# Performance work log

Measured on AMD Instinct MI355X. Metric: run time of the kernel, lower is better.

Reference implementation:

```python
import jax, jax.numpy as jnp
import numpy as np

B, T, E, H = 8, 1024, 1024, 16
D = E // H  # head_dim = 64


def setup_inputs() -> dict:
    key = jax.random.key(0)
    ks = jax.random.split(key, 11)
    s = 1.0 / np.sqrt(E)
    inp = {
        'query': jax.random.normal(ks[0], (B, T, E), jnp.float32),
        'key': jax.random.normal(ks[1], (B, T, E), jnp.float32),
        'value': jax.random.normal(ks[2], (B, T, E), jnp.float32),
        'Wq': jax.random.uniform(ks[3], (E, E), jnp.float32, -s, s),
        'bq': jax.random.uniform(ks[4], (E,), jnp.float32, -s, s),
        'Wk': jax.random.uniform(ks[5], (E, E), jnp.float32, -s, s),
        'bk': jax.random.uniform(ks[6], (E,), jnp.float32, -s, s),
        'Wv': jax.random.uniform(ks[7], (E, E), jnp.float32, -s, s),
        'bv': jax.random.uniform(ks[8], (E,), jnp.float32, -s, s),
        'Wo': jax.random.uniform(ks[9], (E, E), jnp.float32, -s, s),
        'bo': jax.random.uniform(ks[10], (E,), jnp.float32, -s, s),
    }
    return inp


def reference(query, key, value, Wq, bq, Wk, bk, Wv, bv, Wo, bo):
    scale = np.sqrt(D).astype(np.float32)
    # projections: Linear applies x @ W.T + b (torch convention); W shape (out,in)
    q = (query @ Wq.T + bq).reshape(B, T, H, D).transpose(0, 2, 1, 3)  # (B,H,Tq,D)
    k = (key @ Wk.T + bk).reshape(B, T, H, D).transpose(0, 2, 1, 3)    # (B,H,Tk,D)
    v = (value @ Wv.T + bv).reshape(B, T, H, D).transpose(0, 2, 1, 3)  # (B,H,Tk,D)
    scores = jnp.einsum('bhqd,bhkd->bhqk', q, k) / scale
    attn = jax.nn.softmax(scores, axis=-1)  # dropout = identity (eval)
    out = jnp.einsum('bhqk,bhkd->bhqd', attn, v)
    out = out.transpose(0, 2, 1, 3).reshape(B, T, E)
    return out @ Wo.T + bo
```

## Files before the change

### kernel.cpp

```cpp
#include <hip/hip_runtime.h>
#include <stdint.h>

#define BB 8
#define TT 1024
#define EE 1024
#define HH 16
#define DD 64

typedef __attribute__((ext_vector_type(8))) __bf16 bf16x8;
typedef __attribute__((ext_vector_type(4))) float f32x4;
typedef __attribute__((ext_vector_type(4))) unsigned short ushort4v;
typedef __attribute__((ext_vector_type(4))) unsigned int uint4v;

__device__ __forceinline__ unsigned short f2bf(float f) {
  unsigned int u = __float_as_uint(f);
  u += 0x7fffu + ((u >> 16) & 1u);
  return (unsigned short)(u >> 16);
}

__device__ __forceinline__ unsigned int pk2(float a, float b) {
  return ((unsigned int)f2bf(b) << 16) | (unsigned int)f2bf(a);
}

__device__ __forceinline__ f32x4 mfma_16x16x32(bf16x8 a, bf16x8 b, f32x4 c) {
  return __builtin_amdgcn_mfma_f32_16x16x32_bf16(a, b, c, 0, 0, 0);
}

__device__ __forceinline__ void async_ld16(const unsigned short* g, unsigned short* l) {
  __builtin_amdgcn_global_load_lds(
      (const __attribute__((address_space(1))) void*)g,
      (__attribute__((address_space(3))) void*)l, 16, 0, 0);
}

__global__ __launch_bounds__(256) void cast_all(
    const float* __restrict__ xq, const float* __restrict__ xk, const float* __restrict__ xv,
    const float* __restrict__ wq, const float* __restrict__ wk,
    const float* __restrict__ wv, const float* __restrict__ wo,
    unsigned short* __restrict__ ws) {
  int blk = blockIdx.x;
  const float* src; size_t dstoff; int rel;
  if (blk < 4096)       { src = xq; dstoff = 0;        rel = blk; }
  else if (blk < 8192)  { src = xk; dstoff = 8388608;  rel = blk - 4096; }
  else if (blk < 12288) { src = xv; dstoff = 16777216; rel = blk - 8192; }
  else if (blk < 12800) { src = wq; dstoff = 25165824; rel = blk - 12288; }
  else if (blk < 13312) { src = wk; dstoff = 26214400; rel = blk - 12800; }
  else if (blk < 13824) { src = wv; dstoff = 27262976; rel = blk - 13312; }
  else                  { src = wo; dstoff = 28311552; rel = blk - 13824; }
  size_t base = (size_t)rel * 2048 + (size_t)threadIdx.x * 8;
  float4 a = *(const float4*)(src + base);
  float4 b = *(const float4*)(src + base + 4);
  ushort4v o0, o1;
  o0.x = f2bf(a.x); o0.y = f2bf(a.y); o0.z = f2bf(a.z); o0.w = f2bf(a.w);
  o1.x = f2bf(b.x); o1.y = f2bf(b.y); o1.z = f2bf(b.z); o1.w = f2bf(b.w);
  *(ushort4v*)(ws + dstoff + base) = o0;
  *(ushort4v*)(ws + dstoff + base + 4) = o1;
}

template <int OMODE, int AMODE>
__global__ __launch_bounds__(256) void gemm_bt(
    const unsigned short* __restrict__ A, const unsigned short* __restrict__ Wm,
    const float* __restrict__ bias, void* __restrict__ Cout, float scale) {
  const int tid = threadIdx.x;
  const int wave = tid >> 6, lane = tid & 63;
  const int quad = lane >> 4, l16 = lane & 15;
  const int wr = wave >> 1, wc = wave & 1;
  const int n0 = blockIdx.x * 128;
  const int m0 = blockIdx.y * 128;

  __shared__ __align__(16) unsigned short As[128 * 64];
  __shared__ __align__(16) unsigned short Bs[128 * 64];

  const unsigned short* Wb = Wm + (size_t)n0 * 1024 +
                             (OMODE == 2 ? (size_t)blockIdx.z * 1048576 : (size_t)0);

  f32x4 acc[4][4];
#pragma unroll
  for (int i = 0; i < 4; ++i)
#pragma unroll
    for (int j = 0; j < 4; ++j) acc[i][j] = (f32x4){0.f, 0.f, 0.f, 0.f};

  const int row_s = tid >> 3, kc_s = (tid & 7) * 8;
  for (int kt = 0; kt < 16; ++kt) {
    const unsigned short* Akt;
    if (AMODE == 0)
      Akt = A + (size_t)m0 * 1024 + kt * 64;
    else
      Akt = A + (size_t)(m0 >> 10) * 1048576 + (size_t)kt * 65536 + (size_t)(m0 & 1023) * 64;
    const unsigned short* Wkt = Wb + kt * 64;
    const int arow = (AMODE == 0) ? 1024 : 64;
#pragma unroll
    for (int i = 0; i < 4; ++i) {
      int g = i * 256 + tid;
      int row = row_s + i * 32, kc = kc_s;
      async_ld16(Akt + (size_t)row * arow + kc, As + g * 8);
      async_ld16(Wkt + (size_t)row * 1024 + kc, Bs + g * 8);
    }
    __syncthreads();
#pragma unroll
    for (int ks = 0; ks < 2; ++ks) {
      bf16x8 af[4], bfv[4];
      int ko = ks * 32 + quad * 8;
#pragma unroll
      for (int i = 0; i < 4; ++i)
        af[i] = *(const bf16x8*)(As + (wr * 64 + i * 16 + l16) * 64 + ko);
#pragma unroll
      for (int j = 0; j < 4; ++j)
        bfv[j] = *(const bf16x8*)(Bs + (wc * 64 + j * 16 + l16) * 64 + ko);
#pragma unroll
      for (int i = 0; i < 4; ++i)
#pragma unroll
        for (int j = 0; j < 4; ++j) acc[i][j] = mfma_16x16x32(af[i], bfv[j], acc[i][j]);
    }
    __syncthreads();
  }

  if (OMODE == 2) {
    unsigned short* Co = (unsigned short*)Cout;
    size_t zoff = (size_t)blockIdx.z * 1048576;
    const int nxor = ((((l16 >> 2) + 1) & 2) ? 12 : 0);
#pragma unroll
    for (int i = 0; i < 4; ++i)
#pragma unroll
      for (int r = 0; r < 4; ++r) {
        int m = m0 + wr * 64 + i * 16 + quad * 4 + r;
        float bm = bias[m];
#pragma unroll
        for (int j = 0; j < 4; ++j) {
          int n = (n0 + wc * 64 + j * 16 + l16) ^ nxor;
          Co[zoff + (size_t)m * 1024 + n] = f2bf(acc[i][j][r] + bm);
        }
      }
  } else {
#pragma unroll
    for (int j = 0; j < 4; ++j) {
      int n = n0 + wc * 64 + j * 16 + l16;
      float bn = bias[n];
#pragma unroll
      for (int i = 0; i < 4; ++i)
#pragma unroll
        for (int r = 0; r < 4; ++r) {
          int m = m0 + wr * 64 + i * 16 + quad * 4 + r;
          float v = acc[i][j][r] + bn;
          if (OMODE == 0) {
            ((float*)Cout)[(size_t)m * 1024 + n] = v;
          } else {
            v *= scale;
            int b = m >> 10, t = m & 1023, h = n >> 6, d = n & 63;
            ((unsigned short*)Cout)[((size_t)((b << 4) + h) * 1024 + t) * 64 + d] = f2bf(v);
          }
        }
    }
  }
}

__global__ __launch_bounds__(256) void attn(
    const unsigned short* __restrict__ Q,
    const unsigned short* __restrict__ K,
    const unsigned short* __restrict__ Vt,
    unsigned short* __restrict__ O) {
  const int bh = blockIdx.x;
  const int tid = threadIdx.x;
  const int wave = tid >> 6, lane = tid & 63;
  const int quad = lane >> 4, l16 = lane & 15;
  const int q0 = blockIdx.y * 64 + wave * 16;
  const size_t bhTD = (size_t)bh * (TT * DD);
  const unsigned short* Qb = Q + bhTD;
  const unsigned short* Kb = K + bhTD;
  const unsigned short* Vb = Vt + bhTD;

  __shared__ __align__(16) unsigned short Ks[64 * 64];
  __shared__ __align__(16) unsigned short Vs[64 * 64];

  bf16x8 q_lo = *(const bf16x8*)(Qb + (size_t)(q0 + l16) * 64 + quad * 8);
  bf16x8 q_hi = *(const bf16x8*)(Qb + (size_t)(q0 + l16) * 64 + 32 + quad * 8);

  f32x4 o_acc[4];
#pragma unroll
  for (int dd = 0; dd < 4; ++dd) o_acc[dd] = (f32x4){0.f, 0.f, 0.f, 0.f};
  float psum = 0.f;
  const bool lo_half = (quad < 2);

  const int srow = tid >> 3;
  const int schunk = tid & 7;

  for (int it = 0; it < 16; ++it) {
    const int kv0 = it * 64;
#pragma unroll
    for (int i = 0; i < 2; ++i) {
      int row = srow + i * 32;
      int gc = schunk ^ (row & 7);
      async_ld16(Kb + (size_t)(kv0 + row) * 64 + gc * 8, Ks + (row * 8 + schunk) * 8);
      async_ld16(Vb + (size_t)row * 1024 + kv0 + gc * 8, Vs + (row * 8 + schunk) * 8);
    }
    __syncthreads();
#pragma unroll
    for (int c = 0; c < 2; ++c) {
      const int r0 = c * 32 + l16;
      const int r1 = r0 + 16;
      const int sw = r0 & 7;
      bf16x8 k00 = *(const bf16x8*)(Ks + (r0 * 8 + (quad ^ sw)) * 8);
      bf16x8 k01 = *(const bf16x8*)(Ks + (r0 * 8 + ((quad + 4) ^ sw)) * 8);
      bf16x8 k10 = *(const bf16x8*)(Ks + (r1 * 8 + (quad ^ sw)) * 8);
      bf16x8 k11 = *(const bf16x8*)(Ks + (r1 * 8 + ((quad + 4) ^ sw)) * 8);
      f32x4 f0 = (f32x4){0.f, 0.f, 0.f, 0.f};
      f32x4 f1 = (f32x4){0.f, 0.f, 0.f, 0.f};
      f0 = mfma_16x16x32(k00, q_lo, f0);
      f0 = mfma_16x16x32(k01, q_hi, f0);
      f1 = mfma_16x16x32(k10, q_lo, f1);
      f1 = mfma_16x16x32(k11, q_hi, f1);
      float p0 = __expf(f0[0]), p1 = __expf(f0[1]), p2 = __expf(f0[2]), p3 = __expf(f0[3]);
      float p4 = __expf(f1[0]), p5 = __expf(f1[1]), p6 = __expf(f1[2]), p7 = __expf(f1[3]);
      psum += ((p0 + p1) + (p2 + p3)) + ((p4 + p5) + (p6 + p7));
      unsigned int u01 = pk2(p0, p1), u23 = pk2(p2, p3);
      unsigned int u45 = pk2(p4, p5), u67 = pk2(p6, p7);
      unsigned int pu01 = __shfl_xor(u01, 32), pu23 = __shfl_xor(u23, 32);
      unsigned int pu45 = __shfl_xor(u45, 32), pu67 = __shfl_xor(u67, 32);
      uint4v av;
      av.x = lo_half ? u01 : pu45;
      av.y = lo_half ? u23 : pu67;
      av.z = lo_half ? pu01 : u45;
      av.w = lo_half ? pu23 : u67;
      bf16x8 ap = __builtin_bit_cast(bf16x8, av);
#pragma unroll
      for (int dd = 0; dd < 4; ++dd) {
        int vr = dd * 16 + l16;
        bf16x8 bv = *(const bf16x8*)(Vs + (vr * 8 + ((c * 4 + quad) ^ (vr & 7))) * 8);
        o_acc[dd] = mfma_16x16x32(ap, bv, o_acc[dd]);
      }
    }
    __syncthreads();
  }
  psum += __shfl_xor(psum, 16);
  psum += __shfl_xor(psum, 32);
  float inv = 1.f / psum;
#pragma unroll
  for (int r = 0; r < 4; ++r) {
    float invr = __shfl(inv, (lane & 48) | (quad * 4 + r));
    int trow = q0 + quad * 4 + r;
#pragma unroll
    for (int dd = 0; dd < 4; ++dd)
      O[bhTD + (size_t)trow * 64 + dd * 16 + l16] = f2bf(o_acc[dd][r] * invr);
  }
}

extern "C" void kernel_launch(void* const* d_in, const int* in_sizes, int n_in,
                              void* d_out, int out_size, void* d_ws, size_t ws_size,
                              hipStream_t stream) {
  const float* xq = (const float*)d_in[0];
  const float* xk = (const float*)d_in[1];
  const float* xv = (const float*)d_in[2];
  const float* Wq = (const float*)d_in[3];
  const float* bq = (const float*)d_in[4];
  const float* Wk = (const float*)d_in[5];
  const float* bk = (const float*)d_in[6];
  const float* Wv = (const float*)d_in[7];
  const float* bv = (const float*)d_in[8];
  const float* Wo = (const float*)d_in[9];
  const float* bo = (const float*)d_in[10];

  unsigned short* ws = (unsigned short*)d_ws;
  unsigned short* xq_b = ws;
  unsigned short* xk_b = ws + 8388608;
  unsigned short* xv_b = ws + 16777216;
  unsigned short* wq_b = ws + 25165824;
  unsigned short* wk_b = ws + 26214400;
  unsigned short* wv_b = ws + 27262976;
  unsigned short* wo_b = ws + 28311552;
  unsigned short* Qbuf = ws + 29360128;
  unsigned short* Kbuf = ws + 37748736;
  unsigned short* Vtb  = ws + 46137344;
  unsigned short* Obuf = ws + 54525952;

  cast_all<<<14336, 256, 0, stream>>>(xq, xk, xv, Wq, Wk, Wv, Wo, ws);

  gemm_bt<1, 0><<<dim3(8, 64, 1), 256, 0, stream>>>(xq_b, wq_b, bq, (void*)Qbuf, 0.125f);
  gemm_bt<1, 0><<<dim3(8, 64, 1), 256, 0, stream>>>(xk_b, wk_b, bk, (void*)Kbuf, 1.0f);
  gemm_bt<2, 0><<<dim3(8, 8, 8), 256, 0, stream>>>(wv_b, xv_b, bv, (void*)Vtb, 1.0f);
  attn<<<dim3(128, 16), 256, 0, stream>>>(Qbuf, Kbuf, Vtb, Obuf);
  gemm_bt<0, 1><<<dim3(8, 64, 1), 256, 0, stream>>>(Obuf, wo_b, bo, d_out, 1.0f);
}
```

Measured before the change: 339.2 us.

## Fuse QKV projections into one launch, use exp2 and MFMA row sums

```diff
diff --git a/kernel.cpp b/kernel.cpp
--- a/kernel.cpp
+++ b/kernel.cpp
@@ -6,6 +6,8 @@
 #define EE 1024
 #define HH 16
 #define DD 64
+
+#define L2E8 0.18033688011112042f
 
 typedef __attribute__((ext_vector_type(8))) __bf16 bf16x8;
 typedef __attribute__((ext_vector_type(4))) float f32x4;
@@ -56,10 +58,118 @@
   *(ushort4v*)(ws + dstoff + base + 4) = o1;
 }
 
-template <int OMODE, int AMODE>
-__global__ __launch_bounds__(256) void gemm_bt(
+__global__ __launch_bounds__(256, 3) void fused_proj(
+    const unsigned short* __restrict__ xq, const unsigned short* __restrict__ xk,
+    const unsigned short* __restrict__ xv, const unsigned short* __restrict__ wq,
+    const unsigned short* __restrict__ wk, const unsigned short* __restrict__ wv,
+    const float* __restrict__ bq, const float* __restrict__ bk, const float* __restrict__ bv,
+    unsigned short* __restrict__ Qb, unsigned short* __restrict__ Kb,
+    unsigned short* __restrict__ Vtb) {
+  const int id = blockIdx.x;
+  const int tid = threadIdx.x;
+  const int wave = tid >> 6, lane = tid & 63;
+  const int quad = lane >> 4, l16 = lane & 15;
+  const int wr = wave >> 1, wc = wave & 1;
+
+  const unsigned short *A, *W;
+  const float* bias;
+  int mode, m0, n0;
+  size_t zoff = 0;
+  if (id < 512) {
+    mode = 0; A = xq; W = wq; bias = bq;
+    m0 = (id >> 3) * 128; n0 = (id & 7) * 128;
+  } else if (id < 1024) {
+    int t = id - 512;
+    mode = 1; A = xk; W = wk; bias = bk;
+    m0 = (t >> 3) * 128; n0 = (t & 7) * 128;
+  } else {
+    int t = id - 1024;
+    int z = t >> 6;
+    mode = 2; A = wv; W = xv + (size_t)z * 1048576; bias = bv;
+    m0 = ((t >> 3) & 7) * 128; n0 = (t & 7) * 128;
+    zoff = (size_t)z * 1048576;
+  }
+
+  __shared__ __align__(16) unsigned short As[128 * 64];
+  __shared__ __align__(16) unsigned short Bs[128 * 64];
+
+  const unsigned short* Wb = W + (size_t)n0 * 1024;
+
+  f32x4 acc[4][4];
+#pragma unroll
+  for (int i = 0; i < 4; ++i)
+#pragma unroll
+    for (int j = 0; j < 4; ++j) acc[i][j] = (f32x4){0.f, 0.f, 0.f, 0.f};
+
+  const int row_s = tid >> 3, kc_s = (tid & 7) * 8;
+  for (int kt = 0; kt < 16; ++kt) {
+    const unsigned short* Akt = A + (size_t)m0 * 1024 + kt * 64;
+    const unsigned short* Wkt = Wb + kt * 64;
+#pragma unroll
+    for (int i = 0; i < 4; ++i) {
+      int g = i * 256 + tid;
+      int row = row_s + i * 32;
+      async_ld16(Akt + (size_t)row * 1024 + kc_s, As + g * 8);
+      async_ld16(Wkt + (size_t)row * 1024 + kc_s, Bs + g * 8);
+    }
+    __syncthreads();
+#pragma unroll
+    for (int ks = 0; ks < 2; ++ks) {
+      bf16x8 af[4], bfv[4];
+      int ko = ks * 32 + quad * 8;
+#pragma unroll
+      for (int i = 0; i < 4; ++i)
+        af[i] = *(const bf16x8*)(As + (wr * 64 + i * 16 + l16) * 64 + ko);
+#pragma unroll
+      for (int j = 0; j < 4; ++j)
+        bfv[j] = *(const bf16x8*)(Bs + (wc * 64 + j * 16 + l16) * 64 + ko);
+#pragma unroll
+      for (int i = 0; i < 4; ++i)
+#pragma unroll
+        for (int j = 0; j < 4; ++j) acc[i][j] = mfma_16x16x32(af[i], bfv[j], acc[i][j]);
+    }
+    __syncthreads();
+  }
+
+  if (mode == 2) {
+    size_t base = zoff;
+    const int nxor = ((((l16 >> 2) + 1) & 2) ? 12 : 0);
+#pragma unroll
+    for (int i = 0; i < 4; ++i)
+#pragma unroll
+      for (int r = 0; r < 4; ++r) {
+        int m = m0 + wr * 64 + i * 16 + quad * 4 + r;
+        float bm = bias[m];
+#pragma unroll
+        for (int j = 0; j < 4; ++j) {
+          int n = (n0 + wc * 64 + j * 16 + l16) ^ nxor;
+          Vtb[base + (size_t)m * 1024 + n] = f2bf(acc[i][j][r] + bm);
+        }
+      }
+  } else {
+    unsigned short* Out = (mode == 0) ? Qb : Kb;
+    const float scale = (mode == 0) ? L2E8 : 1.0f;
+#pragma unroll
+    for (int j = 0; j < 4; ++j) {
+      int n = n0 + wc * 64 + j * 16 + l16;
+      float bn = bias[n];
+      int h = n >> 6, d = n & 63;
+#pragma unroll
+      for (int i = 0; i < 4; ++i)
+#pragma unroll
+        for (int r = 0; r < 4; ++r) {
+          int m = m0 + wr * 64 + i * 16 + quad * 4 + r;
+          int b = m >> 10, t = m & 1023;
+          float v = (acc[i][j][r] + bn) * scale;
+          Out[((size_t)((b << 4) + h) * 1024 + t) * 64 + d] = f2bf(v);
+        }
+    }
+  }
+}
+
+__global__ __launch_bounds__(256) void gemm_out(
     const unsigned short* __restrict__ A, const unsigned short* __restrict__ Wm,
-    const float* __restrict__ bias, void* __restrict__ Cout, float scale) {
+    const float* __restrict__ bias, float* __restrict__ Cout) {
   const int tid = threadIdx.x;
   const int wave = tid >> 6, lane = tid & 63;
   const int quad = lane >> 4, l16 = lane & 15;
@@ -70,8 +180,7 @@
   __shared__ __align__(16) unsigned short As[128 * 64];
   __shared__ __align__(16) unsigned short Bs[128 * 64];
 
-  const unsigned short* Wb = Wm + (size_t)n0 * 1024 +
-                             (OMODE == 2 ? (size_t)blockIdx.z * 1048576 : (size_t)0);
+  const unsigned short* Wb = Wm + (size_t)n0 * 1024;
 
   f32x4 acc[4][4];
 #pragma unroll
@@ -81,19 +190,15 @@
 
   const int row_s = tid >> 3, kc_s = (tid & 7) * 8;
   for (int kt = 0; kt < 16; ++kt) {
-    const unsigned short* Akt;
-    if (AMODE == 0)
-      Akt = A + (size_t)m0 * 1024 + kt * 64;
-    else
-      Akt = A + (size_t)(m0 >> 10) * 1048576 + (size_t)kt * 65536 + (size_t)(m0 & 1023) * 64;
+    const unsigned short* Akt =
+        A + (size_t)(m0 >> 10) * 1048576 + (size_t)kt * 65536 + (size_t)(m0 & 1023) * 64;
     const unsigned short* Wkt = Wb + kt * 64;
-    const int arow = (AMODE == 0) ? 1024 : 64;
 #pragma unroll
     for (int i = 0; i < 4; ++i) {
       int g = i * 256 + tid;
-      int row = row_s + i * 32, kc = kc_s;
-      async_ld16(Akt + (size_t)row * arow + kc, As + g * 8);
-      async_ld16(Wkt + (size_t)row * 1024 + kc, Bs + g * 8);
+      int row = row_s + i * 32;
+      async_ld16(Akt + (size_t)row * 64 + kc_s, As + g * 8);
+      async_ld16(Wkt + (size_t)row * 1024 + kc_s, Bs + g * 8);
     }
     __syncthreads();
 #pragma unroll
@@ -114,42 +219,17 @@
     __syncthreads();
   }
 
-  if (OMODE == 2) {
-    unsigned short* Co = (unsigned short*)Cout;
-    size_t zoff = (size_t)blockIdx.z * 1048576;
-    const int nxor = ((((l16 >> 2) + 1) & 2) ? 12 : 0);
+#pragma unroll
+  for (int j = 0; j < 4; ++j) {
+    int n = n0 + wc * 64 + j * 16 + l16;
+    float bn = bias[n];
 #pragma unroll
     for (int i = 0; i < 4; ++i)
 #pragma unroll
       for (int r = 0; r < 4; ++r) {
         int m = m0 + wr * 64 + i * 16 + quad * 4 + r;
-        float bm = bias[m];
-#pragma unroll
-        for (int j = 0; j < 4; ++j) {
-          int n = (n0 + wc * 64 + j * 16 + l16) ^ nxor;
-          Co[zoff + (size_t)m * 1024 + n] = f2bf(acc[i][j][r] + bm);
-        }
+        Cout[(size_t)m * 1024 + n] = acc[i][j][r] + bn;
       }
-  } else {
-#pragma unroll
-    for (int j = 0; j < 4; ++j) {
-      int n = n0 + wc * 64 + j * 16 + l16;
-      float bn = bias[n];
-#pragma unroll
-      for (int i = 0; i < 4; ++i)
-#pragma unroll
-        for (int r = 0; r < 4; ++r) {
-          int m = m0 + wr * 64 + i * 16 + quad * 4 + r;
-          float v = acc[i][j][r] + bn;
-          if (OMODE == 0) {
-            ((float*)Cout)[(size_t)m * 1024 + n] = v;
-          } else {
-            v *= scale;
-            int b = m >> 10, t = m & 1023, h = n >> 6, d = n & 63;
-            ((unsigned short*)Cout)[((size_t)((b << 4) + h) * 1024 + t) * 64 + d] = f2bf(v);
-          }
-        }
-    }
   }
 }
 
@@ -174,10 +254,13 @@
   bf16x8 q_lo = *(const bf16x8*)(Qb + (size_t)(q0 + l16) * 64 + quad * 8);
   bf16x8 q_hi = *(const bf16x8*)(Qb + (size_t)(q0 + l16) * 64 + 32 + quad * 8);
 
+  uint4v ou; ou.x = ou.y = ou.z = ou.w = 0x3F803F80u;
+  const bf16x8 ones = __builtin_bit_cast(bf16x8, ou);
+
   f32x4 o_acc[4];
 #pragma unroll
   for (int dd = 0; dd < 4; ++dd) o_acc[dd] = (f32x4){0.f, 0.f, 0.f, 0.f};
-  float psum = 0.f;
+  f32x4 acc5 = (f32x4){0.f, 0.f, 0.f, 0.f};
   const bool lo_half = (quad < 2);
 
   const int srow = tid >> 3;
@@ -208,9 +291,10 @@
       f0 = mfma_16x16x32(k01, q_hi, f0);
       f1 = mfma_16x16x32(k10, q_lo, f1);
       f1 = mfma_16x16x32(k11, q_hi, f1);
-      float p0 = __expf(f0[0]), p1 = __expf(f0[1]), p2 = __expf(f0[2]), p3 = __expf(f0[3]);
-      float p4 = __expf(f1[0]), p5 = __expf(f1[1]), p6 = __expf(f1[2]), p7 = __expf(f1[3]);
-      psum += ((p0 + p1) + (p2 + p3)) + ((p4 + p5) + (p6 + p7));
+      float p0 = __builtin_amdgcn_exp2f(f0[0]), p1 = __builtin_amdgcn_exp2f(f0[1]);
+      float p2 = __builtin_amdgcn_exp2f(f0[2]), p3 = __builtin_amdgcn_exp2f(f0[3]);
+      float p4 = __builtin_amdgcn_exp2f(f1[0]), p5 = __builtin_amdgcn_exp2f(f1[1]);
+      float p6 = __builtin_amdgcn_exp2f(f1[2]), p7 = __builtin_amdgcn_exp2f(f1[3]);
       unsigned int u01 = pk2(p0, p1), u23 = pk2(p2, p3);
       unsigned int u45 = pk2(p4, p5), u67 = pk2(p6, p7);
       unsigned int pu01 = __shfl_xor(u01, 32), pu23 = __shfl_xor(u23, 32);
@@ -221,6 +305,7 @@
       av.z = lo_half ? pu01 : u45;
       av.w = lo_half ? pu23 : u67;
       bf16x8 ap = __builtin_bit_cast(bf16x8, av);
+      acc5 = mfma_16x16x32(ap, ones, acc5);
 #pragma unroll
       for (int dd = 0; dd < 4; ++dd) {
         int vr = dd * 16 + l16;
@@ -230,12 +315,9 @@
     }
     __syncthreads();
   }
-  psum += __shfl_xor(psum, 16);
-  psum += __shfl_xor(psum, 32);
-  float inv = 1.f / psum;
 #pragma unroll
   for (int r = 0; r < 4; ++r) {
-    float invr = __shfl(inv, (lane & 48) | (quad * 4 + r));
+    float invr = 1.f / acc5[r];
     int trow = q0 + quad * 4 + r;
 #pragma unroll
     for (int dd = 0; dd < 4; ++dd)
@@ -273,9 +355,8 @@
 
   cast_all<<<14336, 256, 0, stream>>>(xq, xk, xv, Wq, Wk, Wv, Wo, ws);
 
-  gemm_bt<1, 0><<<dim3(8, 64, 1), 256, 0, stream>>>(xq_b, wq_b, bq, (void*)Qbuf, 0.125f);
-  gemm_bt<1, 0><<<dim3(8, 64, 1), 256, 0, stream>>>(xk_b, wk_b, bk, (void*)Kbuf, 1.0f);
-  gemm_bt<2, 0><<<dim3(8, 8, 8), 256, 0, stream>>>(wv_b, xv_b, bv, (void*)Vtb, 1.0f);
+  fused_proj<<<1536, 256, 0, stream>>>(xq_b, xk_b, xv_b, wq_b, wk_b, wv_b,
+                                       bq, bk, bv, Qbuf, Kbuf, Vtb);
   attn<<<dim3(128, 16), 256, 0, stream>>>(Qbuf, Kbuf, Vtb, Obuf);
-  gemm_bt<0, 1><<<dim3(8, 64, 1), 256, 0, stream>>>(Obuf, wo_b, bo, d_out, 1.0f);
-}
+  gemm_out<<<dim3(8, 64), 256, 0, stream>>>(Obuf, wo_b, bo, (float*)d_out);
+}
```

Result: faster. 320.6 us (-5.5%).
